# Kernel optimization log

Hardware: AMD Instinct MI355X
Metric: run time of the kernel (lower is better)

Reference implementation:

```python
import jax, jax.numpy as jnp
import numpy as np

N, DEG, D_IN, D_HID = 50000, 16, 963, 256


def setup_inputs() -> dict:
    key = jax.random.key(0)
    ks = jax.random.split(key, 8)
    s = 0.02
    neighbours = jax.random.randint(ks[0], (N, DEG), 0, N)
    shape_features = jax.random.normal(ks[1], (N, D_IN), dtype=jnp.float32)
    # layer 0: D_IN -> D_HID; layers 1..13 (stacked): D_HID -> D_HID; extra: D_HID -> 3
    W_self0 = jax.random.normal(ks[2], (D_IN, D_HID), dtype=jnp.float32) * s
    W_neigh0 = jax.random.normal(ks[3], (D_IN, D_HID), dtype=jnp.float32) * s
    b0 = jnp.zeros((D_HID,), jnp.float32)
    W_self = jax.random.normal(ks[4], (13, D_HID, D_HID), dtype=jnp.float32) * s
    W_neigh = jax.random.normal(ks[5], (13, D_HID, D_HID), dtype=jnp.float32) * s
    b = jnp.zeros((13, D_HID), jnp.float32)
    W_extra = jax.random.normal(ks[6], (D_HID, 3), dtype=jnp.float32) * s
    b_extra = jnp.zeros((3,), jnp.float32)
    return {
        "neighbours": neighbours,
        "shape_features": shape_features,
        "W_self0": W_self0, "W_neigh0": W_neigh0, "b0": b0,
        "W_self": W_self, "W_neigh": W_neigh, "b": b,
        "W_extra": W_extra, "b_extra": b_extra,
    }


def _gcn(x, neighbours, Ws, Wn, bias):
    # gather neighbour features [N, DEG, D] and sum-aggregate, plus self transform
    agg = jnp.take(x, neighbours, axis=0).sum(axis=1)
    return x @ Ws + agg @ Wn + bias


def reference(neighbours, shape_features, W_self0, W_neigh0, b0, W_self, W_neigh, b, W_extra, b_extra):
    x = jax.nn.relu(_gcn(shape_features, neighbours, W_self0, W_neigh0, b0))
    for i in range(6):  # 6 residual blocks of 2 GCN layers each
        temp = x
        x = jax.nn.relu(_gcn(x, neighbours, W_self[2 * i], W_neigh[2 * i], b[2 * i]))
        x = jax.nn.relu(_gcn(x, neighbours, W_self[2 * i + 1], W_neigh[2 * i + 1], b[2 * i + 1]))
        x = (temp + x) / 2
    x = jax.nn.relu(_gcn(x, neighbours, W_self[12], W_neigh[12], b[12]))
    coordinates = x @ W_extra + b_extra  # extra layer called without neighbours -> linear
    return (x, coordinates)
```

## Files before the change

### kernel.cpp

```cpp
#include <hip/hip_runtime.h>
#include <hip/hip_bf16.h>
#include <hip/hip_fp16.h>
#include <stdint.h>

#define NNODES 50000
#define NPAD   50048
#define DEG    16
#define DIN    963
#define K0PAD  992
#define DHID   256
#define SCALE  (1.0f / 1024.0f)
#define ISCALE 1024.0f

typedef __attribute__((ext_vector_type(4))) float    f32x4;
typedef __attribute__((ext_vector_type(8))) _Float16 f16x8;
typedef __attribute__((ext_vector_type(4))) _Float16 f16x4;

typedef const __attribute__((address_space(1))) void GV;
typedef __attribute__((address_space(3))) void LV;

__device__ __forceinline__ void gl2lds16(const void* g, void* l) {
    __builtin_amdgcn_global_load_lds((GV*)g, (LV*)l, 16, 0, 0);
}

__device__ __forceinline__ int xcd_swz(int bid, int nwg) {
    const int q = nwg >> 3, r_ = nwg & 7, xc = bid & 7;
    return (xc < r_ ? xc * (q + 1) : r_ * (q + 1) + (xc - r_) * q) + (bid >> 3);
}

__global__ __launch_bounds__(256) void gemm_dual0(
    const _Float16* __restrict__ A, int K,
    const _Float16* __restrict__ Wp,
    _Float16* __restrict__ ys, _Float16* __restrict__ yn)
{
    __shared__ _Float16 lds[2][2][4096];

    const int tid  = threadIdx.x;
    const int w    = tid >> 6;
    const int lane = tid & 63;

    const int wgid = xcd_swz(blockIdx.x, gridDim.x);
    const int bm   = (wgid >> 2) << 7;
    const int nb   = (wgid & 3) << 7;

    const int KT = K >> 5;

    auto stage = [&](int s, int kt) {
        const int k0 = kt << 5;
#pragma unroll
        for (int i = 0; i < 2; ++i) {
            const int j   = w + (i << 2);
            const int c   = (j << 6) + lane;
            const int row = c & 127;
            const int k8  = (c >> 7) << 3;
            gl2lds16(A  + (size_t)(bm + row) * K + k0 + k8, &lds[s][0][(size_t)j << 9]);
            gl2lds16(Wp + (size_t)(nb + row) * K + k0 + k8, &lds[s][1][(size_t)j << 9]);
        }
    };

    const int wm = (w >> 1) << 6;
    const int wn = (w & 1) << 6;
    const int lr = lane & 15;
    const int kh = lane >> 4;

    f32x4 acc[4][4] = {};

    stage(0, 0);
    __syncthreads();
    int cur = 0;
    for (int kt = 0; kt < KT; ++kt) {
        if (kt + 1 < KT) stage(cur ^ 1, kt + 1);
        f16x8 a[4], b[4];
#pragma unroll
        for (int mi = 0; mi < 4; ++mi)
            a[mi] = *(const f16x8*)&lds[cur][0][((kh << 7) + wm + (mi << 4) + lr) << 3];
#pragma unroll
        for (int ni = 0; ni < 4; ++ni)
            b[ni] = *(const f16x8*)&lds[cur][1][((kh << 7) + wn + (ni << 4) + lr) << 3];
#pragma unroll
        for (int mi = 0; mi < 4; ++mi)
#pragma unroll
            for (int ni = 0; ni < 4; ++ni)
                acc[mi][ni] = __builtin_amdgcn_mfma_f32_16x16x32_f16(a[mi], b[ni], acc[mi][ni], 0, 0, 0);
        __syncthreads();
        cur ^= 1;
    }

    _Float16* C = (nb < 256) ? ys : yn;
    const int cb = (nb & 255) + wn;
#pragma unroll
    for (int mi = 0; mi < 4; ++mi) {
        const size_t rbase = (size_t)(bm + wm + (mi << 4) + (kh << 2)) << 8;
#pragma unroll
        for (int ni = 0; ni < 4; ++ni) {
            const int col = cb + (ni << 4) + lr;
#pragma unroll
            for (int r = 0; r < 4; ++r)
                C[rbase + ((size_t)r << 8) + col] = (_Float16)acc[mi][ni][r];
        }
    }
}

template<int FINAL>
__global__ __launch_bounds__(256) void gemm_hidden(
    const _Float16* __restrict__ X, const _Float16* __restrict__ AG,
    const _Float16* __restrict__ Wp,
    const float* __restrict__ bias,
    const _Float16* __restrict__ res,
    _Float16* __restrict__ outh, float* __restrict__ outf)
{
    __shared__ _Float16 lds[2][2][4096];

    const int tid  = threadIdx.x;
    const int w    = tid >> 6;
    const int lane = tid & 63;

    const int wgid = xcd_swz(blockIdx.x, gridDim.x);
    const int bm   = (wgid >> 1) << 7;
    const int nb   = (wgid & 1) << 7;

    auto stage = [&](int s, int kt) {
        const _Float16* Asrc = (kt < 8) ? X : AG;
        const int ka = (kt & 7) << 5;
#pragma unroll
        for (int i = 0; i < 2; ++i) {
            const int j   = w + (i << 2);
            const int c   = (j << 6) + lane;
            const int row = c & 127;
            const int k8  = (c >> 7) << 3;
            gl2lds16(Asrc + ((size_t)(bm + row) << 8) + ka + k8, &lds[s][0][(size_t)j << 9]);
            gl2lds16(Wp + (size_t)(nb + row) * 512 + (kt << 5) + k8, &lds[s][1][(size_t)j << 9]);
        }
    };

    const int wm = (w >> 1) << 6;
    const int wn = (w & 1) << 6;
    const int lr = lane & 15;
    const int kh = lane >> 4;

    f32x4 acc[4][4] = {};

    stage(0, 0);
    __syncthreads();
    int cur = 0;
    for (int kt = 0; kt < 16; ++kt) {
        if (kt + 1 < 16) stage(cur ^ 1, kt + 1);
        f16x8 a[4], b[4];
#pragma unroll
        for (int mi = 0; mi < 4; ++mi)
            a[mi] = *(const f16x8*)&lds[cur][0][((kh << 7) + wm + (mi << 4) + lr) << 3];
#pragma unroll
        for (int ni = 0; ni < 4; ++ni)
            b[ni] = *(const f16x8*)&lds[cur][1][((kh << 7) + wn + (ni << 4) + lr) << 3];
#pragma unroll
        for (int mi = 0; mi < 4; ++mi)
#pragma unroll
            for (int ni = 0; ni < 4; ++ni)
                acc[mi][ni] = __builtin_amdgcn_mfma_f32_16x16x32_f16(a[mi], b[ni], acc[mi][ni], 0, 0, 0);
        __syncthreads();
        cur ^= 1;
    }

#pragma unroll
    for (int mi = 0; mi < 4; ++mi) {
        const int grow0 = bm + wm + (mi << 4) + (kh << 2);
#pragma unroll
        for (int ni = 0; ni < 4; ++ni) {
            const int col = nb + wn + (ni << 4) + lr;
            const float bcol = bias[col] * SCALE;
#pragma unroll
            for (int r = 0; r < 4; ++r) {
                const int grow = grow0 + r;
                float s = acc[mi][ni][r] + bcol;
                s = fmaxf(s, 0.f);
                if (res) s = ((float)res[((size_t)grow << 8) + col] + s) * 0.5f;
                if (FINAL) {
                    if (grow < NNODES) outf[((size_t)grow << 8) + col] = s * ISCALE;
                } else {
                    outh[((size_t)grow << 8) + col] = (_Float16)s;
                }
            }
        }
    }
}

__global__ __launch_bounds__(256) void gather16(
    const _Float16* __restrict__ X, const int* __restrict__ nbr,
    _Float16* __restrict__ agg)
{
    const int idx = blockIdx.x * 256 + threadIdx.x;
    const int r   = idx >> 5;
    const int c8  = (idx & 31) << 3;
    const int rr  = (r < NNODES) ? r : (NNODES - 1);
    const int4* np = (const int4*)(nbr + rr * DEG);
    const int4 q0 = np[0], q1 = np[1], q2 = np[2], q3 = np[3];

    f16x8 v[16];
#define LD16(slot, n) v[slot] = *(const f16x8*)(X + ((size_t)(n) << 8) + c8)
    LD16(0,  q0.x); LD16(1,  q0.y); LD16(2,  q0.z); LD16(3,  q0.w);
    LD16(4,  q1.x); LD16(5,  q1.y); LD16(6,  q1.z); LD16(7,  q1.w);
    LD16(8,  q2.x); LD16(9,  q2.y); LD16(10, q2.z); LD16(11, q2.w);
    LD16(12, q3.x); LD16(13, q3.y); LD16(14, q3.z); LD16(15, q3.w);
#undef LD16
    const f16x8 s0 = ((v[0] + v[1]) + (v[2] + v[3])) + ((v[4] + v[5]) + (v[6] + v[7]));
    const f16x8 s1 = ((v[8] + v[9]) + (v[10] + v[11])) + ((v[12] + v[13]) + (v[14] + v[15]));
    const f16x8 o  = s0 + s1;
    *(f16x8*)(agg + ((size_t)r << 8) + c8) = o;
}

__global__ __launch_bounds__(256) void combine16(
    const _Float16* __restrict__ ys, const _Float16* __restrict__ yn,
    const int* __restrict__ nbr, const float* __restrict__ bias,
    _Float16* __restrict__ outh)
{
    const int idx = blockIdx.x * 256 + threadIdx.x;
    const int r   = idx >> 5;
    const int c8  = (idx & 31) << 3;
    const int4* np = (const int4*)(nbr + r * DEG);
    const int4 q0 = np[0], q1 = np[1], q2 = np[2], q3 = np[3];

    f16x8 v[16];
#define LD16(slot, n) v[slot] = *(const f16x8*)(yn + ((size_t)(n) << 8) + c8)
    LD16(0,  q0.x); LD16(1,  q0.y); LD16(2,  q0.z); LD16(3,  q0.w);
    LD16(4,  q1.x); LD16(5,  q1.y); LD16(6,  q1.z); LD16(7,  q1.w);
    LD16(8,  q2.x); LD16(9,  q2.y); LD16(10, q2.z); LD16(11, q2.w);
    LD16(12, q3.x); LD16(13, q3.y); LD16(14, q3.z); LD16(15, q3.w);
#undef LD16
    const f16x8 ysv = *(const f16x8*)(ys + ((size_t)r << 8) + c8);
    const float4 b0 = *(const float4*)(bias + c8);
    const float4 b1 = *(const float4*)(bias + c8 + 4);
    const float bb[8] = {b0.x, b0.y, b0.z, b0.w, b1.x, b1.y, b1.z, b1.w};
    f16x8 o;
#pragma unroll
    for (int i = 0; i < 8; ++i) {
        float s = (float)ysv[i] + bb[i] * SCALE;
#pragma unroll
        for (int j = 0; j < 16; ++j) s += (float)v[j][i];
        o[i] = (_Float16)fmaxf(s, 0.f);
    }
    *(f16x8*)(outh + ((size_t)r << 8) + c8) = o;
}

__global__ __launch_bounds__(64) void coords_kernel(
    const float* __restrict__ x, const float* __restrict__ We,
    const float* __restrict__ be, float* __restrict__ out3, int N)
{
    const int n = blockIdx.x;
    const int l = threadIdx.x;
    const float4 xv = *(const float4*)(x + (size_t)n * 256 + l * 4);
    float p0 = 0.f, p1 = 0.f, p2 = 0.f;
    const float xs[4] = {xv.x, xv.y, xv.z, xv.w};
#pragma unroll
    for (int i = 0; i < 4; ++i) {
        const int cidx = l * 4 + i;
        p0 += xs[i] * We[cidx * 3 + 0];
        p1 += xs[i] * We[cidx * 3 + 1];
        p2 += xs[i] * We[cidx * 3 + 2];
    }
#pragma unroll
    for (int off = 32; off > 0; off >>= 1) {
        p0 += __shfl_down(p0, off);
        p1 += __shfl_down(p1, off);
        p2 += __shfl_down(p2, off);
    }
    if (l == 0) {
        out3[(size_t)n * 3 + 0] = p0 + be[0];
        out3[(size_t)n * 3 + 1] = p1 + be[1];
        out3[(size_t)n * 3 + 2] = p2 + be[2];
    }
}

__global__ __launch_bounds__(256) void conv_sf(const float* __restrict__ sf,
                                               _Float16* __restrict__ sfb)
{
    const int idx = blockIdx.x * 256 + threadIdx.x;
    const int row = idx / 124;
    const int k8  = (idx % 124) << 3;
    f16x8 o = {};
    if (row < NNODES) {
#pragma unroll
        for (int i = 0; i < 8; ++i) {
            const int k = k8 + i;
            o[i] = (k < DIN) ? (_Float16)(sf[(size_t)row * DIN + k] * SCALE) : (_Float16)0.f;
        }
    }
    *(f16x8*)(sfb + (size_t)row * K0PAD + k8) = o;
}

__global__ __launch_bounds__(256) void pack_w0(const float* __restrict__ Ws0,
                                               const float* __restrict__ Wn0,
                                               _Float16* __restrict__ Wp0)
{
    const int idx = blockIdx.x * 256 + threadIdx.x;
    const int nn  = idx & 511;
    const int k8  = idx >> 9;
    const float* W = (nn < 256) ? Ws0 : Wn0;
    const int n0 = nn & 255;
    f16x8 o;
#pragma unroll
    for (int i = 0; i < 8; ++i) {
        const int k = (k8 << 3) + i;
        o[i] = (k < DIN) ? (_Float16)W[(size_t)k * 256 + n0] : (_Float16)0.f;
    }
    *(f16x8*)(Wp0 + (size_t)nn * K0PAD + (k8 << 3)) = o;
}

__global__ __launch_bounds__(256) void pack_w2(const float* __restrict__ Ws,
                                               const float* __restrict__ Wn,
                                               _Float16* __restrict__ Wpk2)
{
    const int idx = blockIdx.x * 256 + threadIdx.x;
    const int n   = idx & 255;
    const int k8  = (idx >> 8) & 63;
    const int l   = idx >> 14;
    f16x8 o;
#pragma unroll
    for (int i = 0; i < 8; ++i) {
        const int k = (k8 << 3) + i;
        const float* W = (k < 256) ? Ws : Wn;
        o[i] = (_Float16)W[(size_t)l * 65536 + (k & 255) * 256 + n];
    }
    *(f16x8*)(Wpk2 + (size_t)l * 131072 + (size_t)n * 512 + (k8 << 3)) = o;
}

extern "C" void kernel_launch(void* const* d_in, const int* in_sizes, int n_in,
                              void* d_out, int out_size, void* d_ws, size_t ws_size,
                              hipStream_t stream)
{
    const int*   nbr = (const int*)d_in[0];
    const float* sf  = (const float*)d_in[1];
    const float* Ws0 = (const float*)d_in[2];
    const float* Wn0 = (const float*)d_in[3];
    const float* b0  = (const float*)d_in[4];
    const float* Ws  = (const float*)d_in[5];
    const float* Wn  = (const float*)d_in[6];
    const float* bb  = (const float*)d_in[7];
    const float* We  = (const float*)d_in[8];
    const float* be  = (const float*)d_in[9];
    float* out = (float*)d_out;

    uint8_t* w = (uint8_t*)d_ws;
    _Float16* sfb  = (_Float16*)w;
    _Float16* P    = (_Float16*)w;
    _Float16* Q    = P + (size_t)NPAD * 256;
    _Float16* R    = Q + (size_t)NPAD * 256;
    _Float16* Wpk2 = R + (size_t)NPAD * 256;
    _Float16* Wp0  = (_Float16*)(w + (size_t)NPAD * K0PAD * 2);
    _Float16* ysb  = Wp0 + (size_t)512 * K0PAD;
    _Float16* ynb  = ysb + (size_t)NPAD * 256;
    _Float16* agg  = ysb;

    conv_sf<<<NPAD * 124 / 256, 256, 0, stream>>>(sf, sfb);
    pack_w0<<<512 * 124 / 256, 256, 0, stream>>>(Ws0, Wn0, Wp0);

    gemm_dual0<<<(NPAD / 128) * 4, 256, 0, stream>>>(sfb, K0PAD, Wp0, ysb, ynb);
    pack_w2<<<13 * 64 * 256 / 256, 256, 0, stream>>>(Ws, Wn, Wpk2);
    combine16<<<NNODES * 32 / 256, 256, 0, stream>>>(ysb, ynb, nbr, b0, P);

    const int hg = (NPAD / 128) * 2;
    const int gg = NPAD * 32 / 256;

    _Float16* buf[3] = {P, Q, R};
    int xi = 0;
    for (int t = 0; t < 6; ++t) {
        const int lA = 2 * t, lB = lA + 1;
        _Float16* a = buf[(xi + 1) % 3];
        _Float16* b = buf[(xi + 2) % 3];
        gather16<<<gg, 256, 0, stream>>>(buf[xi], nbr, agg);
        gemm_hidden<0><<<hg, 256, 0, stream>>>(buf[xi], agg, Wpk2 + (size_t)lA * 131072,
                                               bb + lA * 256, nullptr, a, nullptr);
        gather16<<<gg, 256, 0, stream>>>(a, nbr, agg);
        gemm_hidden<0><<<hg, 256, 0, stream>>>(a, agg, Wpk2 + (size_t)lB * 131072,
                                               bb + lB * 256, buf[xi], b, nullptr);
        xi = (xi + 2) % 3;
    }

    gather16<<<gg, 256, 0, stream>>>(buf[xi], nbr, agg);
    gemm_hidden<1><<<hg, 256, 0, stream>>>(buf[xi], agg, Wpk2 + (size_t)12 * 131072,
                                           bb + 12 * 256, nullptr, nullptr, out);

    coords_kernel<<<NNODES, 64, 0, stream>>>(out, We, be, out + (size_t)NNODES * 256, NNODES);
}
```

Measured before the change: 1.706 ms.

## Use triple-buffered LDS pipeline with vmcnt waits in both GEMM kernels

```diff
diff --git a/kernel.cpp b/kernel.cpp
--- a/kernel.cpp
+++ b/kernel.cpp
@@ -28,12 +28,16 @@
     return (xc < r_ ? xc * (q + 1) : r_ * (q + 1) + (xc - r_) * q) + (bid >> 3);
 }
 
+#define PIPE_WAIT(n)  do { asm volatile("s_waitcnt vmcnt(" #n ")" ::: "memory"); } while (0)
+#define SCHED_FENCE() __builtin_amdgcn_sched_barrier(0)
+
 __global__ __launch_bounds__(256) void gemm_dual0(
     const _Float16* __restrict__ A, int K,
     const _Float16* __restrict__ Wp,
     _Float16* __restrict__ ys, _Float16* __restrict__ yn)
 {
-    __shared__ _Float16 lds[2][2][4096];
+    __shared__ _Float16 ldsA[3][4096];
+    __shared__ _Float16 ldsB[3][4096];
 
     const int tid  = threadIdx.x;
     const int w    = tid >> 6;
@@ -53,8 +57,8 @@
             const int c   = (j << 6) + lane;
             const int row = c & 127;
             const int k8  = (c >> 7) << 3;
-            gl2lds16(A  + (size_t)(bm + row) * K + k0 + k8, &lds[s][0][(size_t)j << 9]);
-            gl2lds16(Wp + (size_t)(nb + row) * K + k0 + k8, &lds[s][1][(size_t)j << 9]);
+            gl2lds16(A  + (size_t)(bm + row) * K + k0 + k8, &ldsA[s][(size_t)j << 9]);
+            gl2lds16(Wp + (size_t)(nb + row) * K + k0 + k8, &ldsB[s][(size_t)j << 9]);
         }
     };
 
@@ -66,24 +70,31 @@
     f32x4 acc[4][4] = {};
 
     stage(0, 0);
-    __syncthreads();
+    stage(1, 1);
     int cur = 0;
     for (int kt = 0; kt < KT; ++kt) {
-        if (kt + 1 < KT) stage(cur ^ 1, kt + 1);
+        if (kt + 1 < KT) PIPE_WAIT(4);
+        else             PIPE_WAIT(0);
+        SCHED_FENCE();
+        __builtin_amdgcn_s_barrier();
+        SCHED_FENCE();
+        if (kt + 2 < KT) {
+            const int s2 = (cur == 0) ? 2 : cur - 1;
+            stage(s2, kt + 2);
+        }
         f16x8 a[4], b[4];
 #pragma unroll
         for (int mi = 0; mi < 4; ++mi)
-            a[mi] = *(const f16x8*)&lds[cur][0][((kh << 7) + wm + (mi << 4) + lr) << 3];
+            a[mi] = *(const f16x8*)&ldsA[cur][((kh << 7) + wm + (mi << 4) + lr) << 3];
 #pragma unroll
         for (int ni = 0; ni < 4; ++ni)
-            b[ni] = *(const f16x8*)&lds[cur][1][((kh << 7) + wn + (ni << 4) + lr) << 3];
+            b[ni] = *(const f16x8*)&ldsB[cur][((kh << 7) + wn + (ni << 4) + lr) << 3];
 #pragma unroll
         for (int mi = 0; mi < 4; ++mi)
 #pragma unroll
             for (int ni = 0; ni < 4; ++ni)
                 acc[mi][ni] = __builtin_amdgcn_mfma_f32_16x16x32_f16(a[mi], b[ni], acc[mi][ni], 0, 0, 0);
-        __syncthreads();
-        cur ^= 1;
+        cur = (cur == 2) ? 0 : cur + 1;
     }
 
     _Float16* C = (nb < 256) ? ys : yn;
@@ -109,7 +120,8 @@
     const _Float16* __restrict__ res,
     _Float16* __restrict__ outh, float* __restrict__ outf)
 {
-    __shared__ _Float16 lds[2][2][4096];
+    __shared__ _Float16 ldsA[3][4096];
+    __shared__ _Float16 ldsB[3][4096];
 
     const int tid  = threadIdx.x;
     const int w    = tid >> 6;
@@ -128,8 +140,8 @@
             const int c   = (j << 6) + lane;
             const int row = c & 127;
             const int k8  = (c >> 7) << 3;
-            gl2lds16(Asrc + ((size_t)(bm + row) << 8) + ka + k8, &lds[s][0][(size_t)j << 9]);
-            gl2lds16(Wp + (size_t)(nb + row) * 512 + (kt << 5) + k8, &lds[s][1][(size_t)j << 9]);
+            gl2lds16(Asrc + ((size_t)(bm + row) << 8) + ka + k8, &ldsA[s][(size_t)j << 9]);
+            gl2lds16(Wp + (size_t)(nb + row) * 512 + (kt << 5) + k8, &ldsB[s][(size_t)j << 9]);
         }
     };
 
@@ -141,24 +153,32 @@
     f32x4 acc[4][4] = {};
 
     stage(0, 0);
-    __syncthreads();
+    stage(1, 1);
     int cur = 0;
+#pragma unroll
     for (int kt = 0; kt < 16; ++kt) {
-        if (kt + 1 < 16) stage(cur ^ 1, kt + 1);
+        if (kt < 15) PIPE_WAIT(4);
+        else         PIPE_WAIT(0);
+        SCHED_FENCE();
+        __builtin_amdgcn_s_barrier();
+        SCHED_FENCE();
+        if (kt + 2 < 16) {
+            const int s2 = (cur == 0) ? 2 : cur - 1;
+            stage(s2, kt + 2);
+        }
         f16x8 a[4], b[4];
 #pragma unroll
         for (int mi = 0; mi < 4; ++mi)
-            a[mi] = *(const f16x8*)&lds[cur][0][((kh << 7) + wm + (mi << 4) + lr) << 3];
+            a[mi] = *(const f16x8*)&ldsA[cur][((kh << 7) + wm + (mi << 4) + lr) << 3];
 #pragma unroll
         for (int ni = 0; ni < 4; ++ni)
-            b[ni] = *(const f16x8*)&lds[cur][1][((kh << 7) + wn + (ni << 4) + lr) << 3];
+            b[ni] = *(const f16x8*)&ldsB[cur][((kh << 7) + wn + (ni << 4) + lr) << 3];
 #pragma unroll
         for (int mi = 0; mi < 4; ++mi)
 #pragma unroll
             for (int ni = 0; ni < 4; ++ni)
                 acc[mi][ni] = __builtin_amdgcn_mfma_f32_16x16x32_f16(a[mi], b[ni], acc[mi][ni], 0, 0, 0);
-        __syncthreads();
-        cur ^= 1;
+        cur = (cur == 2) ? 0 : cur + 1;
     }
 
 #pragma unroll
```

Result: no change. 1.708 ms (+0.1%).

## Overlap self-GEMM with neighbour gather in one launch, split hidden GEMM

Applied to the files above, without the earlier changes.

```diff
diff --git a/kernel.cpp b/kernel.cpp
--- a/kernel.cpp
+++ b/kernel.cpp
@@ -11,6 +11,8 @@
 #define DHID   256
 #define SCALE  (1.0f / 1024.0f)
 #define ISCALE 1024.0f
+#define GEMM_BLKS 782
+#define GATH_BLKS 6256
 
 typedef __attribute__((ext_vector_type(4))) float    f32x4;
 typedef __attribute__((ext_vector_type(8))) _Float16 f16x8;
@@ -81,7 +83,7 @@
         for (int mi = 0; mi < 4; ++mi)
 #pragma unroll
             for (int ni = 0; ni < 4; ++ni)
-                acc[mi][ni] = __builtin_amdgcn_mfma_f32_16x16x32_f16(a[mi], b[ni], acc[mi][ni], 0, 0, 0);
+                acc[mi][ni] = __builtin_amdgcn_mfma_f32_16x16x32_f16(b[ni], a[mi], acc[mi][ni], 0, 0, 0);
         __syncthreads();
         cur ^= 1;
     }
@@ -90,46 +92,64 @@
     const int cb = (nb & 255) + wn;
 #pragma unroll
     for (int mi = 0; mi < 4; ++mi) {
-        const size_t rbase = (size_t)(bm + wm + (mi << 4) + (kh << 2)) << 8;
+        const int m = bm + wm + (mi << 4) + lr;
 #pragma unroll
         for (int ni = 0; ni < 4; ++ni) {
-            const int col = cb + (ni << 4) + lr;
-#pragma unroll
-            for (int r = 0; r < 4; ++r)
-                C[rbase + ((size_t)r << 8) + col] = (_Float16)acc[mi][ni][r];
-        }
-    }
-}
-
-template<int FINAL>
-__global__ __launch_bounds__(256) void gemm_hidden(
-    const _Float16* __restrict__ X, const _Float16* __restrict__ AG,
-    const _Float16* __restrict__ Wp,
-    const float* __restrict__ bias,
-    const _Float16* __restrict__ res,
-    _Float16* __restrict__ outh, float* __restrict__ outf)
+            const int col0 = cb + (ni << 4) + (kh << 2);
+            f16x4 o;
+#pragma unroll
+            for (int r = 0; r < 4; ++r) o[r] = (_Float16)acc[mi][ni][r];
+            *(f16x4*)(C + ((size_t)m << 8) + col0) = o;
+        }
+    }
+}
+
+__global__ __launch_bounds__(256) void self_gather(
+    const _Float16* __restrict__ X, const int* __restrict__ nbr,
+    const _Float16* __restrict__ W,
+    _Float16* __restrict__ ys, _Float16* __restrict__ agg)
 {
     __shared__ _Float16 lds[2][2][4096];
 
-    const int tid  = threadIdx.x;
+    const int tid = threadIdx.x;
+
+    if (blockIdx.x >= GEMM_BLKS) {
+        const int idx = (blockIdx.x - GEMM_BLKS) * 256 + tid;
+        const int r   = idx >> 5;
+        const int c8  = (idx & 31) << 3;
+        const int rr  = (r < NNODES) ? r : (NNODES - 1);
+        const int4* np = (const int4*)(nbr + rr * DEG);
+        const int4 q0 = np[0], q1 = np[1], q2 = np[2], q3 = np[3];
+        f16x8 v[16];
+#define LD16(slot, n) v[slot] = *(const f16x8*)(X + ((size_t)(n) << 8) + c8)
+        LD16(0,  q0.x); LD16(1,  q0.y); LD16(2,  q0.z); LD16(3,  q0.w);
+        LD16(4,  q1.x); LD16(5,  q1.y); LD16(6,  q1.z); LD16(7,  q1.w);
+        LD16(8,  q2.x); LD16(9,  q2.y); LD16(10, q2.z); LD16(11, q2.w);
+        LD16(12, q3.x); LD16(13, q3.y); LD16(14, q3.z); LD16(15, q3.w);
+#undef LD16
+        const f16x8 s0 = ((v[0] + v[1]) + (v[2] + v[3])) + ((v[4] + v[5]) + (v[6] + v[7]));
+        const f16x8 s1 = ((v[8] + v[9]) + (v[10] + v[11])) + ((v[12] + v[13]) + (v[14] + v[15]));
+        const f16x8 o  = s0 + s1;
+        *(f16x8*)(agg + ((size_t)r << 8) + c8) = o;
+        return;
+    }
+
     const int w    = tid >> 6;
     const int lane = tid & 63;
-
-    const int wgid = xcd_swz(blockIdx.x, gridDim.x);
+    const int wgid = xcd_swz(blockIdx.x, GEMM_BLKS);
     const int bm   = (wgid >> 1) << 7;
     const int nb   = (wgid & 1) << 7;
 
     auto stage = [&](int s, int kt) {
-        const _Float16* Asrc = (kt < 8) ? X : AG;
-        const int ka = (kt & 7) << 5;
+        const int k0 = kt << 5;
 #pragma unroll
         for (int i = 0; i < 2; ++i) {
             const int j   = w + (i << 2);
             const int c   = (j << 6) + lane;
             const int row = c & 127;
             const int k8  = (c >> 7) << 3;
-            gl2lds16(Asrc + ((size_t)(bm + row) << 8) + ka + k8, &lds[s][0][(size_t)j << 9]);
-            gl2lds16(Wp + (size_t)(nb + row) * 512 + (kt << 5) + k8, &lds[s][1][(size_t)j << 9]);
+            gl2lds16(X + (((size_t)(bm + row)) << 8) + k0 + k8, &lds[s][0][(size_t)j << 9]);
+            gl2lds16(W + ((size_t)(nb + row) << 9) + k0 + k8, &lds[s][1][(size_t)j << 9]);
         }
     };
 
@@ -143,8 +163,9 @@
     stage(0, 0);
     __syncthreads();
     int cur = 0;
-    for (int kt = 0; kt < 16; ++kt) {
-        if (kt + 1 < 16) stage(cur ^ 1, kt + 1);
+#pragma unroll
+    for (int kt = 0; kt < 8; ++kt) {
+        if (kt + 1 < 8) stage(cur ^ 1, kt + 1);
         f16x8 a[4], b[4];
 #pragma unroll
         for (int mi = 0; mi < 4; ++mi)
@@ -156,56 +177,116 @@
         for (int mi = 0; mi < 4; ++mi)
 #pragma unroll
             for (int ni = 0; ni < 4; ++ni)
-                acc[mi][ni] = __builtin_amdgcn_mfma_f32_16x16x32_f16(a[mi], b[ni], acc[mi][ni], 0, 0, 0);
+                acc[mi][ni] = __builtin_amdgcn_mfma_f32_16x16x32_f16(b[ni], a[mi], acc[mi][ni], 0, 0, 0);
         __syncthreads();
         cur ^= 1;
     }
 
 #pragma unroll
     for (int mi = 0; mi < 4; ++mi) {
-        const int grow0 = bm + wm + (mi << 4) + (kh << 2);
+        const int m = bm + wm + (mi << 4) + lr;
 #pragma unroll
         for (int ni = 0; ni < 4; ++ni) {
-            const int col = nb + wn + (ni << 4) + lr;
-            const float bcol = bias[col] * SCALE;
-#pragma unroll
-            for (int r = 0; r < 4; ++r) {
-                const int grow = grow0 + r;
-                float s = acc[mi][ni][r] + bcol;
-                s = fmaxf(s, 0.f);
-                if (res) s = ((float)res[((size_t)grow << 8) + col] + s) * 0.5f;
-                if (FINAL) {
-                    if (grow < NNODES) outf[((size_t)grow << 8) + col] = s * ISCALE;
-                } else {
-                    outh[((size_t)grow << 8) + col] = (_Float16)s;
+            const int col0 = nb + wn + (ni << 4) + (kh << 2);
+            f16x4 o;
+#pragma unroll
+            for (int r = 0; r < 4; ++r) o[r] = (_Float16)acc[mi][ni][r];
+            *(f16x4*)(ys + ((size_t)m << 8) + col0) = o;
+        }
+    }
+}
+
+template<int FINAL>
+__global__ __launch_bounds__(256) void neigh_gemm(
+    const _Float16* __restrict__ AG, const _Float16* __restrict__ W,
+    const _Float16* __restrict__ ysb, const float* __restrict__ bias,
+    const _Float16* __restrict__ res,
+    _Float16* __restrict__ outh, float* __restrict__ outf)
+{
+    __shared__ _Float16 lds[2][2][4096];
+
+    const int tid  = threadIdx.x;
+    const int w    = tid >> 6;
+    const int lane = tid & 63;
+    const int wgid = xcd_swz(blockIdx.x, gridDim.x);
+    const int bm   = (wgid >> 1) << 7;
+    const int nb   = (wgid & 1) << 7;
+
+    auto stage = [&](int s, int kt) {
+        const int k0 = kt << 5;
+#pragma unroll
+        for (int i = 0; i < 2; ++i) {
+            const int j   = w + (i << 2);
+            const int c   = (j << 6) + lane;
+            const int row = c & 127;
+            const int k8  = (c >> 7) << 3;
+            gl2lds16(AG + (((size_t)(bm + row)) << 8) + k0 + k8, &lds[s][0][(size_t)j << 9]);
+            gl2lds16(W + ((size_t)(nb + row) << 9) + 256 + k0 + k8, &lds[s][1][(size_t)j << 9]);
+        }
+    };
+
+    const int wm = (w >> 1) << 6;
+    const int wn = (w & 1) << 6;
+    const int lr = lane & 15;
+    const int kh = lane >> 4;
+
+    f32x4 acc[4][4] = {};
+
+    stage(0, 0);
+    __syncthreads();
+    int cur = 0;
+#pragma unroll
+    for (int kt = 0; kt < 8; ++kt) {
+        if (kt + 1 < 8) stage(cur ^ 1, kt + 1);
+        f16x8 a[4], b[4];
+#pragma unroll
+        for (int mi = 0; mi < 4; ++mi)
+            a[mi] = *(const f16x8*)&lds[cur][0][((kh << 7) + wm + (mi << 4) + lr) << 3];
+#pragma unroll
+        for (int ni = 0; ni < 4; ++ni)
+            b[ni] = *(const f16x8*)&lds[cur][1][((kh << 7) + wn + (ni << 4) + lr) << 3];
+#pragma unroll
+        for (int mi = 0; mi < 4; ++mi)
+#pragma unroll
+            for (int ni = 0; ni < 4; ++ni)
+                acc[mi][ni] = __builtin_amdgcn_mfma_f32_16x16x32_f16(b[ni], a[mi], acc[mi][ni], 0, 0, 0);
+        __syncthreads();
+        cur ^= 1;
+    }
+
+#pragma unroll
+    for (int mi = 0; mi < 4; ++mi) {
+        const int m = bm + wm + (mi << 4) + lr;
+        const size_t mb = (size_t)m << 8;
+#pragma unroll
+        for (int ni = 0; ni < 4; ++ni) {
+            const int col0 = nb + wn + (ni << 4) + (kh << 2);
+            const float4 bv = *(const float4*)(bias + col0);
+            const f16x4 yv = *(const f16x4*)(ysb + mb + col0);
+            float s0 = fmaxf(acc[mi][ni][0] + (float)yv[0] + bv.x * SCALE, 0.f);
+            float s1 = fmaxf(acc[mi][ni][1] + (float)yv[1] + bv.y * SCALE, 0.f);
+            float s2 = fmaxf(acc[mi][ni][2] + (float)yv[2] + bv.z * SCALE, 0.f);
+            float s3 = fmaxf(acc[mi][ni][3] + (float)yv[3] + bv.w * SCALE, 0.f);
+            if (res) {
+                const f16x4 rv = *(const f16x4*)(res + mb + col0);
+                s0 = ((float)rv[0] + s0) * 0.5f;
+                s1 = ((float)rv[1] + s1) * 0.5f;
+                s2 = ((float)rv[2] + s2) * 0.5f;
+                s3 = ((float)rv[3] + s3) * 0.5f;
+            }
+            if (FINAL) {
+                if (m < NNODES) {
+                    float4 o = make_float4(s0 * ISCALE, s1 * ISCALE, s2 * ISCALE, s3 * ISCALE);
+                    *(float4*)(outf + mb + col0) = o;
                 }
+            } else {
+                f16x4 o;
+                o[0] = (_Float16)s0; o[1] = (_Float16)s1;
+                o[2] = (_Float16)s2; o[3] = (_Float16)s3;
+                *(f16x4*)(outh + mb + col0) = o;
             }
         }
     }
-}
-
-__global__ __launch_bounds__(256) void gather16(
-    const _Float16* __restrict__ X, const int* __restrict__ nbr,
-    _Float16* __restrict__ agg)
-{
-    const int idx = blockIdx.x * 256 + threadIdx.x;
-    const int r   = idx >> 5;
-    const int c8  = (idx & 31) << 3;
-    const int rr  = (r < NNODES) ? r : (NNODES - 1);
-    const int4* np = (const int4*)(nbr + rr * DEG);
-    const int4 q0 = np[0], q1 = np[1], q2 = np[2], q3 = np[3];
-
-    f16x8 v[16];
-#define LD16(slot, n) v[slot] = *(const f16x8*)(X + ((size_t)(n) << 8) + c8)
-    LD16(0,  q0.x); LD16(1,  q0.y); LD16(2,  q0.z); LD16(3,  q0.w);
-    LD16(4,  q1.x); LD16(5,  q1.y); LD16(6,  q1.z); LD16(7,  q1.w);
-    LD16(8,  q2.x); LD16(9,  q2.y); LD16(10, q2.z); LD16(11, q2.w);
-    LD16(12, q3.x); LD16(13, q3.y); LD16(14, q3.z); LD16(15, q3.w);
-#undef LD16
-    const f16x8 s0 = ((v[0] + v[1]) + (v[2] + v[3])) + ((v[4] + v[5]) + (v[6] + v[7]));
-    const f16x8 s1 = ((v[8] + v[9]) + (v[10] + v[11])) + ((v[12] + v[13]) + (v[14] + v[15]));
-    const f16x8 o  = s0 + s1;
-    *(f16x8*)(agg + ((size_t)r << 8) + c8) = o;
 }
 
 __global__ __launch_bounds__(256) void combine16(
@@ -343,12 +424,12 @@
     _Float16* sfb  = (_Float16*)w;
     _Float16* P    = (_Float16*)w;
     _Float16* Q    = P + (size_t)NPAD * 256;
-    _Float16* R    = Q + (size_t)NPAD * 256;
-    _Float16* Wpk2 = R + (size_t)NPAD * 256;
+    _Float16* Wpk2 = Q + (size_t)NPAD * 256;
     _Float16* Wp0  = (_Float16*)(w + (size_t)NPAD * K0PAD * 2);
     _Float16* ysb  = Wp0 + (size_t)512 * K0PAD;
     _Float16* ynb  = ysb + (size_t)NPAD * 256;
-    _Float16* agg  = ysb;
+    _Float16* AG   = ysb;
+    _Float16* YS   = ynb;
 
     conv_sf<<<NPAD * 124 / 256, 256, 0, stream>>>(sf, sfb);
     pack_w0<<<512 * 124 / 256, 256, 0, stream>>>(Ws0, Wn0, Wp0);
@@ -357,27 +438,26 @@
     pack_w2<<<13 * 64 * 256 / 256, 256, 0, stream>>>(Ws, Wn, Wpk2);
     combine16<<<NNODES * 32 / 256, 256, 0, stream>>>(ysb, ynb, nbr, b0, P);
 
-    const int hg = (NPAD / 128) * 2;
-    const int gg = NPAD * 32 / 256;
-
-    _Float16* buf[3] = {P, Q, R};
-    int xi = 0;
+    const int ag = GEMM_BLKS + GATH_BLKS;
+
     for (int t = 0; t < 6; ++t) {
         const int lA = 2 * t, lB = lA + 1;
-        _Float16* a = buf[(xi + 1) % 3];
-        _Float16* b = buf[(xi + 2) % 3];
-        gather16<<<gg, 256, 0, stream>>>(buf[xi], nbr, agg);
-        gemm_hidden<0><<<hg, 256, 0, stream>>>(buf[xi], agg, Wpk2 + (size_t)lA * 131072,
-                                               bb + lA * 256, nullptr, a, nullptr);
-        gather16<<<gg, 256, 0, stream>>>(a, nbr, agg);
-        gemm_hidden<0><<<hg, 256, 0, stream>>>(a, agg, Wpk2 + (size_t)lB * 131072,
-                                               bb + lB * 256, buf[xi], b, nullptr);
-        xi = (xi + 2) % 3;
-    }
-
-    gather16<<<gg, 256, 0, stream>>>(buf[xi], nbr, agg);
-    gemm_hidden<1><<<hg, 256, 0, stream>>>(buf[xi], agg, Wpk2 + (size_t)12 * 131072,
-                                           bb + 12 * 256, nullptr, nullptr, out);
+        const _Float16* WA = Wpk2 + (size_t)lA * 131072;
+        const _Float16* WB = Wpk2 + (size_t)lB * 131072;
+        self_gather<<<ag, 256, 0, stream>>>(P, nbr, WA, YS, AG);
+        neigh_gemm<0><<<GEMM_BLKS, 256, 0, stream>>>(AG, WA, YS, bb + lA * 256,
+                                                     nullptr, Q, nullptr);
+        self_gather<<<ag, 256, 0, stream>>>(Q, nbr, WB, YS, AG);
+        neigh_gemm<0><<<GEMM_BLKS, 256, 0, stream>>>(AG, WB, YS, bb + lB * 256,
+                                                     P, P, nullptr);
+    }
+
+    {
+        const _Float16* WL = Wpk2 + (size_t)12 * 131072;
+        self_gather<<<ag, 256, 0, stream>>>(P, nbr, WL, YS, AG);
+        neigh_gemm<1><<<GEMM_BLKS, 256, 0, stream>>>(AG, WL, YS, bb + 12 * 256,
+                                                     nullptr, nullptr, out);
+    }
 
     coords_kernel<<<NNODES, 64, 0, stream>>>(out, We, be, out + (size_t)NNODES * 256, NNODES);
 }
```

After: 1.752 ms. 1.03x slower.
